# Kernel optimization log

Measured on AMD Instinct MI355X. Metric: run time of the kernel, lower is better.

Reference implementation:

```python
import jax, jax.numpy as jnp
import numpy as np

THETA = 10000.0
D_K = 128
MAX_SEQ_LEN = 8192
BATCH, HEADS, SEQ = 4, 16, 4096


def setup_inputs() -> dict:
    key = jax.random.key(0)
    kx, = jax.random.split(key, 1)
    x = jax.random.normal(kx, (BATCH, HEADS, SEQ, D_K), dtype=jnp.float32)
    token_positions = jnp.arange(SEQ, dtype=jnp.int32)  # broadcast over batch dims
    # Precompute the same angles the torch module bakes into its block-diag
    # rotation matrices: angle[i, k] = i / theta ** (2k / d_k)
    k = jnp.arange(D_K // 2, dtype=jnp.float32)
    inv_freq = THETA ** (-2.0 * k / D_K)                      # [d_k/2]
    pos = jnp.arange(MAX_SEQ_LEN, dtype=jnp.float32)          # [max_seq_len]
    angles = pos[:, None] * inv_freq[None, :]                 # [max_seq_len, d_k/2]
    cos_table = jnp.cos(angles)
    sin_table = jnp.sin(angles)
    return {"x": x, "token_positions": token_positions,
            "cos_table": cos_table, "sin_table": sin_table}


def reference(x, token_positions, cos_table, sin_table):
    # Gather per-position cos/sin: (..., seq, d_k/2). Mathematically identical
    # to gathering the [d_k, d_k] block-diag rotation matrix and doing a matvec,
    # since each 2x2 block rotates an interleaved pair (x[2k], x[2k+1]).
    c = cos_table[token_positions]
    s = sin_table[token_positions]
    xp = x.reshape(x.shape[:-1] + (D_K // 2, 2))   # (..., seq, d_k/2, 2)
    x1, x2 = xp[..., 0], xp[..., 1]
    o1 = c * x1 - s * x2
    o2 = s * x1 + c * x2
    return jnp.stack((o1, o2), axis=-1).reshape(x.shape)
```

## Files before the change

### kernel.cpp

```cpp
#include <hip/hip_runtime.h>


typedef float f4 __attribute__((ext_vector_type(4)));
typedef float f2 __attribute__((ext_vector_type(2)));

constexpr int SEQ        = 4096;
constexpr int D_K        = 128;
constexpr int F4_PER_ROW = D_K / 4;
constexpr int BLOCK      = 256;
constexpr int GRID       = 2048;

__global__ __launch_bounds__(BLOCK) void rope_kernel(
    const f4* __restrict__ x,
    const int* __restrict__ tok_pos,
    const f2* __restrict__ cos_t,
    const f2* __restrict__ sin_t,
    f4*       __restrict__ out,
    const int n4)
{
    const int tid    = blockIdx.x * BLOCK + threadIdx.x;
    const int stride = GRID * BLOCK;

    const int within = tid & (F4_PER_ROW - 1);
    const int s      = (tid >> 5) & (SEQ - 1);
    const int p      = tok_pos[s];
    const f2 c  = cos_t[p * F4_PER_ROW + within];
    const f2 sn = sin_t[p * F4_PER_ROW + within];

    for (int k = tid; k < n4; k += 4 * stride) {
        f4 a0 = __builtin_nontemporal_load(&x[k]);
        f4 a1 = __builtin_nontemporal_load(&x[k + stride]);
        f4 a2 = __builtin_nontemporal_load(&x[k + 2 * stride]);
        f4 a3 = __builtin_nontemporal_load(&x[k + 3 * stride]);

        f4 o0, o1, o2, o3;
        o0.x = c.x * a0.x - sn.x * a0.y;  o0.y = sn.x * a0.x + c.x * a0.y;
        o0.z = c.y * a0.z - sn.y * a0.w;  o0.w = sn.y * a0.z + c.y * a0.w;
        o1.x = c.x * a1.x - sn.x * a1.y;  o1.y = sn.x * a1.x + c.x * a1.y;
        o1.z = c.y * a1.z - sn.y * a1.w;  o1.w = sn.y * a1.z + c.y * a1.w;
        o2.x = c.x * a2.x - sn.x * a2.y;  o2.y = sn.x * a2.x + c.x * a2.y;
        o2.z = c.y * a2.z - sn.y * a2.w;  o2.w = sn.y * a2.z + c.y * a2.w;
        o3.x = c.x * a3.x - sn.x * a3.y;  o3.y = sn.x * a3.x + c.x * a3.y;
        o3.z = c.y * a3.z - sn.y * a3.w;  o3.w = sn.y * a3.z + c.y * a3.w;

        __builtin_nontemporal_store(o0, &out[k]);
        __builtin_nontemporal_store(o1, &out[k + stride]);
        __builtin_nontemporal_store(o2, &out[k + 2 * stride]);
        __builtin_nontemporal_store(o3, &out[k + 3 * stride]);
    }
}

extern "C" void kernel_launch(void* const* d_in, const int* in_sizes, int n_in,
                              void* d_out, int out_size, void* d_ws, size_t ws_size,
                              hipStream_t stream) {
    const f4*  x       = (const f4*)d_in[0];
    const int* tok_pos = (const int*)d_in[1];
    const f2*  cos_t   = (const f2*)d_in[2];
    const f2*  sin_t   = (const f2*)d_in[3];
    f4*        out     = (f4*)d_out;

    const int n4 = out_size / 4;
    rope_kernel<<<GRID, BLOCK, 0, stream>>>(x, tok_pos, cos_t, sin_t, out, n4);
}
```

Before: 231.9 us.

## Replace grid-stride loop with one-shot blocks and drop nontemporal hints

Switches from a fixed 2048-block grid-stride loop to a grid sized to the data, where each block handles 4 contiguous strips of 256 float4s and exits. Cos/sin values are now gathered per unrolled element instead of once per thread. Loads and stores lose the nontemporal builtins and become plain accesses. The intent is to reduce per-thread loop overhead and rely on more resident blocks to hide memory latency, at the cost of extra table reads and a possible loss from normal cache policy on streaming data.

```diff
diff --git a/kernel.cpp b/kernel.cpp
--- a/kernel.cpp
+++ b/kernel.cpp
@@ -8,45 +8,40 @@
 constexpr int D_K        = 128;
 constexpr int F4_PER_ROW = D_K / 4;
 constexpr int BLOCK      = 256;
-constexpr int GRID       = 2048;
+constexpr int UNROLL     = 4;
 
 __global__ __launch_bounds__(BLOCK) void rope_kernel(
     const f4* __restrict__ x,
     const int* __restrict__ tok_pos,
     const f2* __restrict__ cos_t,
     const f2* __restrict__ sin_t,
-    f4*       __restrict__ out,
-    const int n4)
+    f4*       __restrict__ out)
 {
-    const int tid    = blockIdx.x * BLOCK + threadIdx.x;
-    const int stride = GRID * BLOCK;
+    const int base = blockIdx.x * (BLOCK * UNROLL) + threadIdx.x;
 
-    const int within = tid & (F4_PER_ROW - 1);
-    const int s      = (tid >> 5) & (SEQ - 1);
-    const int p      = tok_pos[s];
-    const f2 c  = cos_t[p * F4_PER_ROW + within];
-    const f2 sn = sin_t[p * F4_PER_ROW + within];
+    f4 a[UNROLL];
+#pragma unroll
+    for (int u = 0; u < UNROLL; ++u)
+        a[u] = x[base + u * BLOCK];
 
-    for (int k = tid; k < n4; k += 4 * stride) {
-        f4 a0 = __builtin_nontemporal_load(&x[k]);
-        f4 a1 = __builtin_nontemporal_load(&x[k + stride]);
-        f4 a2 = __builtin_nontemporal_load(&x[k + 2 * stride]);
-        f4 a3 = __builtin_nontemporal_load(&x[k + 3 * stride]);
+    const int within = base & (F4_PER_ROW - 1);
+    f2 c[UNROLL], sn[UNROLL];
+#pragma unroll
+    for (int u = 0; u < UNROLL; ++u) {
+        const int s = ((base + u * BLOCK) >> 5) & (SEQ - 1);
+        const int p = tok_pos[s];
+        c[u]  = cos_t[p * F4_PER_ROW + within];
+        sn[u] = sin_t[p * F4_PER_ROW + within];
+    }
 
-        f4 o0, o1, o2, o3;
-        o0.x = c.x * a0.x - sn.x * a0.y;  o0.y = sn.x * a0.x + c.x * a0.y;
-        o0.z = c.y * a0.z - sn.y * a0.w;  o0.w = sn.y * a0.z + c.y * a0.w;
-        o1.x = c.x * a1.x - sn.x * a1.y;  o1.y = sn.x * a1.x + c.x * a1.y;
-        o1.z = c.y * a1.z - sn.y * a1.w;  o1.w = sn.y * a1.z + c.y * a1.w;
-        o2.x = c.x * a2.x - sn.x * a2.y;  o2.y = sn.x * a2.x + c.x * a2.y;
-        o2.z = c.y * a2.z - sn.y * a2.w;  o2.w = sn.y * a2.z + c.y * a2.w;
-        o3.x = c.x * a3.x - sn.x * a3.y;  o3.y = sn.x * a3.x + c.x * a3.y;
-        o3.z = c.y * a3.z - sn.y * a3.w;  o3.w = sn.y * a3.z + c.y * a3.w;
-
-        __builtin_nontemporal_store(o0, &out[k]);
-        __builtin_nontemporal_store(o1, &out[k + stride]);
-        __builtin_nontemporal_store(o2, &out[k + 2 * stride]);
-        __builtin_nontemporal_store(o3, &out[k + 3 * stride]);
+#pragma unroll
+    for (int u = 0; u < UNROLL; ++u) {
+        f4 o;
+        o.x = c[u].x * a[u].x - sn[u].x * a[u].y;
+        o.y = sn[u].x * a[u].x + c[u].x * a[u].y;
+        o.z = c[u].y * a[u].z - sn[u].y * a[u].w;
+        o.w = sn[u].y * a[u].z + c[u].y * a[u].w;
+        out[base + u * BLOCK] = o;
     }
 }
 
@@ -59,6 +54,8 @@
     const f2*  sin_t   = (const f2*)d_in[3];
     f4*        out     = (f4*)d_out;
 
-    const int n4 = out_size / 4;
-    rope_kernel<<<GRID, BLOCK, 0, stream>>>(x, tok_pos, cos_t, sin_t, out, n4);
+    const int n4   = out_size / 4;
+    const int grid = n4 / (BLOCK * UNROLL);
+
+    rope_kernel<<<grid, BLOCK, 0, stream>>>(x, tok_pos, cos_t, sin_t, out);
 }
```

Result: no change. 230.7 us (-0.5%).
